# Optimization experiments

Hardware: AMD Instinct MI355X
Metric: run time of the kernel (lower is better)

The kernel has to match this reference:

```python
import jax, jax.numpy as jnp
import numpy as np

B, NQ, D, H, L, P, FFN = 32, 300, 256, 8, 3, 4, 1024
SPATIAL = [(80, 80), (40, 40), (20, 20)]  # static multi-scale feature shapes (640px, strides 8/16/32)
S = sum(h * w for h, w in SPATIAL)  # 8400
HD = D // H


def _ln(x, g, b, eps=1e-5):
    m = jnp.mean(x, -1, keepdims=True)
    v = jnp.mean((x - m) ** 2, -1, keepdims=True)
    return (x - m) * jax.lax.rsqrt(v + eps) * g + b


def _grid_sample(img, grid):
    # img: (N,C,Hh,Ww); grid: (N,Q,Pp,2) in [-1,1]; bilinear, zeros padding, align_corners=False
    N, C, Hh, Ww = img.shape
    x = (grid[..., 0] + 1.0) * (Ww * 0.5) - 0.5
    y = (grid[..., 1] + 1.0) * (Hh * 0.5) - 0.5
    x0 = jnp.floor(x)
    y0 = jnp.floor(y)
    wx1 = x - x0
    wy1 = y - y0
    x0i = x0.astype(jnp.int32)
    y0i = y0.astype(jnp.int32)
    flat = img.reshape(N, C, Hh * Ww)
    Q, Pp = grid.shape[1], grid.shape[2]

    def corner(xi, yi, w):
        valid = (xi >= 0) & (xi < Ww) & (yi >= 0) & (yi < Hh)
        idx = jnp.clip(yi, 0, Hh - 1) * Ww + jnp.clip(xi, 0, Ww - 1)
        v = jnp.take_along_axis(flat, idx.reshape(N, 1, Q * Pp), axis=2).reshape(N, C, Q, Pp)
        return v * (w * valid)[:, None]

    return (corner(x0i, y0i, (1 - wx1) * (1 - wy1))
            + corner(x0i + 1, y0i, wx1 * (1 - wy1))
            + corner(x0i, y0i + 1, (1 - wx1) * wy1)
            + corner(x0i + 1, y0i + 1, wx1 * wy1))


def setup_inputs() -> dict:
    key = jax.random.key(0)
    ks = iter(jax.random.split(key, 32))
    inp = {
        'hidden_states': jax.random.normal(next(ks), (B, NQ, D), jnp.float32),
        'position_embeddings': jax.random.normal(next(ks), (B, NQ, D), jnp.float32),
        'reference_points': jax.random.uniform(next(ks), (B, NQ, 1, 4), jnp.float32, 0.1, 0.9),
        'encoder_hidden_states': jax.random.normal(next(ks), (B, S, D), jnp.float32),
    }
    for name, shape in [('Wq', (D, D)), ('Wk', (D, D)), ('Wv', (D, D)), ('Wo', (D, D)),
                        ('Woff', (D, H * L * P * 2)), ('Waw', (D, H * L * P)),
                        ('Wval', (D, D)), ('Wout', (D, D)), ('W1', (D, FFN)), ('W2', (FFN, D))]:
        inp[name] = jax.random.normal(next(ks), shape, jnp.float32) * 0.02
    for name, dim in [('bq', D), ('bk', D), ('bv', D), ('bo', D), ('boff', H * L * P * 2),
                      ('baw', H * L * P), ('bval', D), ('bout', D), ('b1', FFN), ('b2', D)]:
        inp[name] = jnp.zeros((dim,), jnp.float32)
    for g, bname in [('ln1_g', 'ln1_b'), ('ln2_g', 'ln2_b'), ('ln3_g', 'ln3_b')]:
        inp[g] = jnp.ones((D,), jnp.float32)
        inp[bname] = jnp.zeros((D,), jnp.float32)
    return inp


def reference(hidden_states, position_embeddings, reference_points, encoder_hidden_states,
              Wq, bq, Wk, bk, Wv, bv, Wo, bo, ln1_g, ln1_b,
              Woff, boff, Waw, baw, Wval, bval, Wout, bout, ln2_g, ln2_b,
              W1, b1, W2, b2, ln3_g, ln3_b):
    hs = hidden_states
    # ---- self attention (pos-embedded q/k, raw v) ----
    hp = hs + position_embeddings
    q = ((hp @ Wq + bq) * (HD ** -0.5)).reshape(B, NQ, H, HD)
    k = (hp @ Wk + bk).reshape(B, NQ, H, HD)
    v = (hs @ Wv + bv).reshape(B, NQ, H, HD)
    attn = jax.nn.softmax(jnp.einsum('bqhd,bkhd->bhqk', q, k), axis=-1)
    sa = jnp.einsum('bhqk,bkhd->bqhd', attn, v).reshape(B, NQ, D) @ Wo + bo
    hs = _ln(hs + sa, ln1_g, ln1_b)
    # ---- multi-scale deformable cross attention ----
    hp = hs + position_embeddings
    value = (encoder_hidden_states @ Wval + bval).reshape(B, S, H, HD)
    off = (hp @ Woff + boff).reshape(B, NQ, H, L, P, 2)
    aw = jax.nn.softmax((hp @ Waw + baw).reshape(B, NQ, H, L * P), axis=-1).reshape(B, NQ, H, L, P)
    ref = reference_points  # (B,NQ,1,4) boxes -> 4-coord branch
    loc = ref[:, :, None, :, None, :2] + off / P * ref[:, :, None, :, None, 2:] * 0.5
    grids = (2.0 * loc - 1.0).transpose(0, 2, 1, 3, 4, 5).reshape(B * H, NQ, L, P, 2)
    start = 0
    samples = []
    for lvl, (hh, ww) in enumerate(SPATIAL):
        v_l = value[:, start:start + hh * ww]  # (B,hw,H,HD)
        start += hh * ww
        v_l = v_l.transpose(0, 2, 3, 1).reshape(B * H, HD, hh, ww)
        samples.append(_grid_sample(v_l, grids[:, :, lvl]))  # (B*H,HD,NQ,P)
    sampled = jnp.stack(samples, axis=3).reshape(B * H, HD, NQ, L * P)
    w = aw.transpose(0, 2, 1, 3, 4).reshape(B * H, 1, NQ, L * P)
    ca = (sampled * w).sum(-1).reshape(B, H * HD, NQ).transpose(0, 2, 1) @ Wout + bout
    hs = _ln(hs + ca, ln2_g, ln2_b)
    # ---- FFN ----
    ff = jax.nn.relu(hs @ W1 + b1) @ W2 + b2
    return _ln(hs + ff, ln3_g, ln3_b)
```

## Files before the change

kernel.cpp:

```cpp
#include <hip/hip_runtime.h>
#include <hip/hip_bf16.h>

typedef unsigned int  uint32;
typedef unsigned short ushort16;
typedef __bf16 bfx8 __attribute__((ext_vector_type(8)));
typedef float  f32x4 __attribute__((ext_vector_type(4)));

typedef __attribute__((address_space(1))) const unsigned int gas_u32;
typedef __attribute__((address_space(3))) unsigned int las_u32;

#define B_   32
#define NQ_  300
#define D_   256
#define H_   8
#define HD_  32
#define L_   3
#define P_   4
#define S_   8400
#define FFN_ 1024
#define M1   (B_*NQ_)
#define MV   (B_*S_)
#define NQP  320
#define NQT  19

__device__ inline ushort16 f2bf(float x) {
  uint32 u = __float_as_uint(x);
  uint32 r = u + 0x7fffu + ((u >> 16) & 1u);
  return (ushort16)(r >> 16);
}
__device__ inline uint32 cvtpk(float lo, float hi) {
  uint32 r; asm("v_cvt_pk_bf16_f32 %0, %1, %2" : "=v"(r) : "v"(lo), "v"(hi)); return r;
}

struct WPrep {
  const float* src[9];
  ushort16*    dst[9];
  int K[9], N[9], Npad[9], tileEnd[9];
  float scale[9];
  const float* wval; ushort16* wvalc;
  const float* bqs;  const float* bks;  float* bqk;
  const float* boffs; const float* baws; float* boffaw;
};

__global__ __launch_bounds__(256) void rt_wprep(WPrep a)
{
  __shared__ float t[32][33];
  int blk = blockIdx.x;
  if (blk < 904) {
    int wi = 0;
    while (blk >= a.tileEnd[wi]) wi++;
    int base = wi ? a.tileEnd[wi - 1] : 0;
    int idx = blk - base;
    int K = a.K[wi], N = a.N[wi];
    int ntx = a.Npad[wi] / 32;
    int n0 = (idx % ntx) * 32, k0 = (idx / ntx) * 32;
    float sc = a.scale[wi];
    const float* W = a.src[wi];
    ushort16* WT = a.dst[wi];
    int c = threadIdx.x & 31, r = threadIdx.x >> 5;
#pragma unroll
    for (int i = 0; i < 4; i++) {
      int nn = n0 + c;
      t[r + i * 8][c] = (nn < N) ? W[(size_t)(k0 + r + i * 8) * N + nn] : 0.f;
    }
    __syncthreads();
#pragma unroll
    for (int i = 0; i < 4; i++)
      WT[(size_t)(n0 + r + i * 8) * K + k0 + c] = f2bf(t[c][r + i * 8] * sc);
  } else if (blk < 936) {
    int gid = (blk - 904) * 256 + threadIdx.x;
    int c = gid >> 8, n = gid & 255;
    const float* W = a.wval;
    uint4 u;
    u.x = (uint32)f2bf(W[(c*8+0)*256 + n]) | ((uint32)f2bf(W[(c*8+1)*256 + n]) << 16);
    u.y = (uint32)f2bf(W[(c*8+2)*256 + n]) | ((uint32)f2bf(W[(c*8+3)*256 + n]) << 16);
    u.z = (uint32)f2bf(W[(c*8+4)*256 + n]) | ((uint32)f2bf(W[(c*8+5)*256 + n]) << 16);
    u.w = (uint32)f2bf(W[(c*8+6)*256 + n]) | ((uint32)f2bf(W[(c*8+7)*256 + n]) << 16);
    *(uint4*)&a.wvalc[(size_t)c * 2048 + n * 8] = u;
  } else if (blk == 936) {
    a.bqk[threadIdx.x] = a.bqs[threadIdx.x] * a.scale[0];
  } else if (blk == 937) {
    a.bqk[256 + threadIdx.x] = a.bks[threadIdx.x];
  } else if (blk == 938) {
    if (threadIdx.x < 192) a.boffaw[threadIdx.x] = a.boffs[threadIdx.x];
  } else {
    if (threadIdx.x < 96) a.boffaw[192 + threadIdx.x] = a.baws[threadIdx.x];
  }
}

__global__ __launch_bounds__(1024, 1) void rt_vgemm(
    const float* __restrict__ A, const ushort16* __restrict__ BC,
    const float* __restrict__ bias, ushort16* __restrict__ Vout)
{
  __shared__ __align__(16) char ldsB[131072];
  const int tid = threadIdx.x;
  const int lane = tid & 63, w = tid >> 6;
  const int l15 = lane & 15, l4 = lane >> 4;

#pragma unroll
  for (int i = 0; i < 8; ++i)
    __builtin_amdgcn_global_load_lds(
        (gas_u32*)(const void*)((const char*)BC + tid * 16 + i * 16384),
        (las_u32*)(void*)(&ldsB[tid * 16 + i * 16384]), 16, 0, 0);
  __syncthreads();

  const int wrow = w * 16 + l15;
  for (int t = blockIdx.x; t < MV / 256; t += 256) {
    const float* Ap = A + ((size_t)t * 256 + wrow) * 256 + l4 * 8;
    f32x4 aA = *(const f32x4*)(Ap);
    f32x4 aB = *(const f32x4*)(Ap + 4);
    f32x4 aC = *(const f32x4*)(Ap + 32);
    f32x4 aD = *(const f32x4*)(Ap + 36);
    f32x4 acc[16];
#pragma unroll
    for (int i = 0; i < 16; ++i) acc[i] = (f32x4){0.f, 0.f, 0.f, 0.f};

#pragma unroll
    for (int tt = 0; tt < 4; ++tt) {
      {
        uint4 u;
        u.x = cvtpk(aA[0], aA[1]); u.y = cvtpk(aA[2], aA[3]);
        u.z = cvtpk(aB[0], aB[1]); u.w = cvtpk(aB[2], aB[3]);
        bfx8 af = __builtin_bit_cast(bfx8, u);
        if (tt < 3) {
          aA = *(const f32x4*)(Ap + (2 * tt + 2) * 32);
          aB = *(const f32x4*)(Ap + (2 * tt + 2) * 32 + 4);
        }
        const char* bp = &ldsB[(2 * tt * 4 + l4) * 4096 + l15 * 16];
#pragma unroll
        for (int ni = 0; ni < 16; ++ni) {
          bfx8 bg = *(const bfx8*)(const void*)(bp + ni * 256);
          acc[ni] = __builtin_amdgcn_mfma_f32_16x16x32_bf16(bg, af, acc[ni], 0, 0, 0);
        }
      }
      {
        uint4 u;
        u.x = cvtpk(aC[0], aC[1]); u.y = cvtpk(aC[2], aC[3]);
        u.z = cvtpk(aD[0], aD[1]); u.w = cvtpk(aD[2], aD[3]);
        bfx8 af = __builtin_bit_cast(bfx8, u);
        if (tt < 3) {
          aC = *(const f32x4*)(Ap + (2 * tt + 3) * 32);
          aD = *(const f32x4*)(Ap + (2 * tt + 3) * 32 + 4);
        }
        const char* bp = &ldsB[((2 * tt + 1) * 4 + l4) * 4096 + l15 * 16];
#pragma unroll
        for (int ni = 0; ni < 16; ++ni) {
          bfx8 bg = *(const bfx8*)(const void*)(bp + ni * 256);
          acc[ni] = __builtin_amdgcn_mfma_f32_16x16x32_bf16(bg, af, acc[ni], 0, 0, 0);
        }
      }
    }
    int row = t * 256 + wrow;
    int bb = row / S_, s = row - bb * S_;
    ushort16* vb = Vout + (((size_t)bb * H_) * S_ + s) * HD_;
#pragma unroll
    for (int ni = 0; ni < 16; ++ni) {
      int col = ni * 16 + l4 * 4;
      f32x4 bv = *(const f32x4*)(bias + col);
      int hh = col >> 5, hd = col & 31;
      uint2 st;
      st.x = cvtpk(acc[ni][0] + bv[0], acc[ni][1] + bv[1]);
      st.y = cvtpk(acc[ni][2] + bv[2], acc[ni][3] + bv[3]);
      *(uint2*)(vb + (size_t)hh * S_ * HD_ + hd) = st;
    }
  }
}

#define GBM 128
#define GBN 128
#define GBK 32
#define LDP 40

__global__ __launch_bounds__(256) void rt_mgemm(
    const float* __restrict__ A, const float* __restrict__ A2,
    const ushort16* __restrict__ BT, const float* __restrict__ bias,
    float* __restrict__ C, float* __restrict__ C2,
    ushort16* __restrict__ Sc, ushort16* __restrict__ Sc2,
    int M, int N, int K, int klen, float scale, int mode)
{
  __shared__ __align__(16) ushort16 As[GBM][LDP];
  __shared__ __align__(16) ushort16 Bs[GBN][LDP];
  const int tid  = threadIdx.x;
  const int lane = tid & 63;
  const int w    = tid >> 6;
  const int wr   = (w >> 1) * 64;
  const int wc   = (w & 1) * 64;
  const int bm   = blockIdx.y * GBM;
  const int bn   = blockIdx.x * GBN;
  const int kz   = blockIdx.z;
  const int kb   = kz * klen;
  const int l15  = lane & 15;
  const int l4   = lane >> 4;

  f32x4 acc[4][4];
#pragma unroll
  for (int i = 0; i < 4; i++)
#pragma unroll
    for (int j = 0; j < 4; j++)
      acc[i][j] = (f32x4){0.f, 0.f, 0.f, 0.f};

  const int arow = tid >> 3, akc = tid & 7;
  const int brow = tid >> 2, bkc = tid & 3;

  for (int k0 = kb; k0 < kb + klen; k0 += GBK) {
#pragma unroll
    for (int i = 0; i < 4; i++) {
      int row = arow + i * 32;
      f32x4 v = *(const f32x4*)(A + (size_t)(bm + row) * K + k0 + akc * 4);
      if (A2) {
        f32x4 v2 = *(const f32x4*)(A2 + (size_t)(bm + row) * K + k0 + akc * 4);
#pragma unroll
        for (int r = 0; r < 4; r++) v[r] += v2[r];
      }
      uint2 u;
      u.x = cvtpk(v.x, v.y);
      u.y = cvtpk(v.z, v.w);
      *(uint2*)(&As[row][akc * 4]) = u;
    }
#pragma unroll
    for (int i = 0; i < 2; i++) {
      int row = brow + i * 64;
      uint4 v = *(const uint4*)(BT + (size_t)(bn + row) * K + k0 + bkc * 8);
      *(uint4*)(&Bs[row][bkc * 8]) = v;
    }
    __syncthreads();

    bfx8 af[4], bg[4];
#pragma unroll
    for (int mi = 0; mi < 4; mi++)
      af[mi] = *(const bfx8*)(&As[wr + mi * 16 + l15][l4 * 8]);
#pragma unroll
    for (int ni = 0; ni < 4; ni++)
      bg[ni] = *(const bfx8*)(&Bs[wc + ni * 16 + l15][l4 * 8]);
#pragma unroll
    for (int mi = 0; mi < 4; mi++)
#pragma unroll
      for (int ni = 0; ni < 4; ni++)
        acc[mi][ni] = __builtin_amdgcn_mfma_f32_16x16x32_bf16(af[mi], bg[ni], acc[mi][ni], 0, 0, 0);
    __syncthreads();
  }

  float* Cp = kz ? C2 : C;
#pragma unroll
  for (int mi = 0; mi < 4; mi++) {
#pragma unroll
    for (int ni = 0; ni < 4; ni++) {
      int col = bn + wc + ni * 16 + l15;
      if (col >= N) continue;
      float bv = kz ? 0.f : bias[col];
#pragma unroll
      for (int r = 0; r < 4; r++) {
        int row = bm + wr + mi * 16 + l4 * 4 + r;
        float vv = (acc[mi][ni][r] + bv) * scale;
        if (mode == 1) vv = fmaxf(vv, 0.f);
        if (mode == 3) {
          int bb = row / NQ_, q = row - bb * NQ_;
          int hh = col >> 5, hd = col & 31;
          Sc[(((size_t)bb * H_ + hh) * NQP + q) * HD_ + hd] = f2bf(vv);
        } else if (mode == 4) {
          int bb = row / NQ_, q = row - bb * NQ_;
          int hh = col >> 5, hd = col & 31;
          ushort16* d = (hh < 8) ? Sc : Sc2;
          d[(((size_t)bb * H_ + (hh & 7)) * NQP + q) * HD_ + hd] = f2bf(vv);
        } else {
          Cp[(size_t)row * N + col] = vv;
        }
      }
    }
  }
}

__global__ __launch_bounds__(256) void rt_vtr(const ushort16* __restrict__ vh,
                                              ushort16* __restrict__ vt)
{
  __shared__ ushort16 t[64][33];
  int bh = blockIdx.x;
  const ushort16* src = vh + (size_t)bh * NQP * HD_;
  ushort16* dst = vt + (size_t)bh * HD_ * NQP;
  int tid = threadIdx.x;
  int lrow = tid >> 2, lc8 = (tid & 3) * 8;
  int ohd = tid >> 3, oq8 = (tid & 7) * 8;
  for (int r0 = 0; r0 < NQP; r0 += 64) {
    uint4 v = *(const uint4*)(src + (size_t)(r0 + lrow) * HD_ + lc8);
    ushort16* tp = &t[lrow][lc8];
    tp[0] = (ushort16)(v.x & 0xffff); tp[1] = (ushort16)(v.x >> 16);
    tp[2] = (ushort16)(v.y & 0xffff); tp[3] = (ushort16)(v.y >> 16);
    tp[4] = (ushort16)(v.z & 0xffff); tp[5] = (ushort16)(v.z >> 16);
    tp[6] = (ushort16)(v.w & 0xffff); tp[7] = (ushort16)(v.w >> 16);
    __syncthreads();
    uint4 o;
    o.x = (uint32)t[oq8 + 0][ohd] | ((uint32)t[oq8 + 1][ohd] << 16);
    o.y = (uint32)t[oq8 + 2][ohd] | ((uint32)t[oq8 + 3][ohd] << 16);
    o.z = (uint32)t[oq8 + 4][ohd] | ((uint32)t[oq8 + 5][ohd] << 16);
    o.w = (uint32)t[oq8 + 6][ohd] | ((uint32)t[oq8 + 7][ohd] << 16);
    *(uint4*)(dst + (size_t)ohd * NQP + r0 + oq8) = o;
    __syncthreads();
  }
}

__global__ __launch_bounds__(256) void rt_fattn(
    const ushort16* __restrict__ qh, const ushort16* __restrict__ kh,
    const ushort16* __restrict__ vt, float* __restrict__ O)
{
  int gw  = blockIdx.x * 4 + (threadIdx.x >> 6);
  int bh  = gw / NQT, qt = gw - bh * NQT;
  int b   = bh >> 3, h = bh & 7;
  int lane = threadIdx.x & 63;
  int l15 = lane & 15, l4 = lane >> 4;
  int kb4 = l4 * 4;
  const ushort16* Qb = qh + (size_t)bh * NQP * HD_;
  const ushort16* Kb = kh + (size_t)bh * NQP * HD_;
  const ushort16* Vb = vt + (size_t)bh * HD_ * NQP;
  int q = qt * 16 + l15;

  bfx8 bgQ = *(const bfx8*)(const void*)(Qb + (size_t)q * HD_ + l4 * 8);
  f32x4 o0 = {0.f,0.f,0.f,0.f}, o1 = {0.f,0.f,0.f,0.f};
  float m = -1e30f, ssum = 0.f;

  for (int k0 = 0; k0 < NQP; k0 += 32) {
    bfx8 afk0 = *(const bfx8*)(const void*)(Kb + (size_t)(k0 + l15) * HD_ + l4 * 8);
    bfx8 afk1 = *(const bfx8*)(const void*)(Kb + (size_t)(k0 + 16 + l15) * HD_ + l4 * 8);
    f32x4 z = {0.f,0.f,0.f,0.f};
    f32x4 s0 = __builtin_amdgcn_mfma_f32_16x16x32_bf16(afk0, bgQ, z, 0, 0, 0);
    f32x4 s1 = __builtin_amdgcn_mfma_f32_16x16x32_bf16(afk1, bgQ, z, 0, 0, 0);
    int ka = k0 + kb4, kbb = k0 + 16 + kb4;
#pragma unroll
    for (int r = 0; r < 4; r++) {
      if (ka  + r >= NQ_) s0[r] = -1e30f;
      if (kbb + r >= NQ_) s1[r] = -1e30f;
    }
    float cm = fmaxf(fmaxf(fmaxf(s0[0], s0[1]), fmaxf(s0[2], s0[3])),
                     fmaxf(fmaxf(s1[0], s1[1]), fmaxf(s1[2], s1[3])));
    cm = fmaxf(cm, __shfl_xor(cm, 16));
    cm = fmaxf(cm, __shfl_xor(cm, 32));
    float nm = fmaxf(m, cm);
    float sc = __expf(m - nm);
    m = nm;
    f32x4 p0, p1;
#pragma unroll
    for (int r = 0; r < 4; r++) { p0[r] = __expf(s0[r] - m); p1[r] = __expf(s1[r] - m); }
    float ls = (p0[0]+p0[1]+p0[2]+p0[3]) + (p1[0]+p1[1]+p1[2]+p1[3]);
    ls += __shfl_xor(ls, 16);
    ls += __shfl_xor(ls, 32);
    ssum = ssum * sc + ls;

    uint32 t0w0 = cvtpk(p0[0], p0[1]);
    uint32 t0w1 = cvtpk(p0[2], p0[3]);
    uint32 t1w0 = cvtpk(p1[0], p1[1]);
    uint32 t1w1 = cvtpk(p1[2], p1[3]);
    int srcA = l15 + 32 * (l4 & 1);
    int srcB = srcA + 16;
    uint32 a00 = __shfl((int)t0w0, srcA), a01 = __shfl((int)t0w1, srcA);
    uint32 b00 = __shfl((int)t0w0, srcB), b01 = __shfl((int)t0w1, srcB);
    uint32 a10 = __shfl((int)t1w0, srcA), a11 = __shfl((int)t1w1, srcA);
    uint32 b10 = __shfl((int)t1w0, srcB), b11 = __shfl((int)t1w1, srcB);
    bool hi = (l4 >= 2);
    uint4 pw;
    pw.x = hi ? a10 : a00;
    pw.y = hi ? a11 : a01;
    pw.z = hi ? b10 : b00;
    pw.w = hi ? b11 : b01;
    bfx8 bgP = __builtin_bit_cast(bfx8, pw);

    bfx8 afv0 = *(const bfx8*)(const void*)(Vb + (size_t)l15 * NQP + k0 + l4 * 8);
    bfx8 afv1 = *(const bfx8*)(const void*)(Vb + (size_t)(16 + l15) * NQP + k0 + l4 * 8);
#pragma unroll
    for (int r = 0; r < 4; r++) { o0[r] *= sc; o1[r] *= sc; }
    o0 = __builtin_amdgcn_mfma_f32_16x16x32_bf16(afv0, bgP, o0, 0, 0, 0);
    o1 = __builtin_amdgcn_mfma_f32_16x16x32_bf16(afv1, bgP, o1, 0, 0, 0);
  }

  if (q < NQ_) {
    float inv = 1.f / ssum;
    float* op = O + ((size_t)(b * NQ_ + q)) * D_ + h * HD_ + kb4;
    f32x4 r0, r1;
#pragma unroll
    for (int r = 0; r < 4; r++) { r0[r] = o0[r] * inv; r1[r] = o1[r] * inv; }
    *(f32x4*)op = r0;
    *(f32x4*)(op + 16) = r1;
  }
}

__global__ __launch_bounds__(256) void rt_ln2(
    const float* __restrict__ X, const float* __restrict__ R1,
    const float* __restrict__ R2,
    const float* __restrict__ g, const float* __restrict__ be,
    float* __restrict__ O, int rows)
{
  int row = blockIdx.x * 4 + (threadIdx.x >> 6);
  int lane = threadIdx.x & 63;
  if (row >= rows) return;
  size_t base = (size_t)row * D_ + lane * 4;
  float4 x = *(const float4*)(X + base);
  float4 r = *(const float4*)(R1 + base);
  float v0 = x.x + r.x, v1 = x.y + r.y, v2 = x.z + r.z, v3 = x.w + r.w;
  if (R2) {
    float4 r2 = *(const float4*)(R2 + base);
    v0 += r2.x; v1 += r2.y; v2 += r2.z; v3 += r2.w;
  }
  float s = v0 + v1 + v2 + v3;
  float sq = v0*v0 + v1*v1 + v2*v2 + v3*v3;
#pragma unroll
  for (int o = 32; o >= 1; o >>= 1) { s += __shfl_xor(s, o); sq += __shfl_xor(sq, o); }
  float mean = s * (1.f / D_);
  float var  = sq * (1.f / D_) - mean * mean;
  float inv  = 1.f / sqrtf(var + 1e-5f);
  int c = lane * 4;
  float4 gv = *(const float4*)(g + c);
  float4 bv = *(const float4*)(be + c);
  float4 o4;
  o4.x = (v0 - mean) * inv * gv.x + bv.x;
  o4.y = (v1 - mean) * inv * gv.y + bv.y;
  o4.z = (v2 - mean) * inv * gv.z + bv.z;
  o4.w = (v3 - mean) * inv * gv.w + bv.w;
  *(float4*)(O + base) = o4;
}

__device__ inline void rt_acc8(const ushort16* p, float wgt, float* acc) {
  uint4 v = *(const uint4*)(const void*)p;
  acc[0] += wgt * __uint_as_float(v.x << 16);
  acc[1] += wgt * __uint_as_float(v.x & 0xffff0000u);
  acc[2] += wgt * __uint_as_float(v.y << 16);
  acc[3] += wgt * __uint_as_float(v.y & 0xffff0000u);
  acc[4] += wgt * __uint_as_float(v.z << 16);
  acc[5] += wgt * __uint_as_float(v.z & 0xffff0000u);
  acc[6] += wgt * __uint_as_float(v.w << 16);
  acc[7] += wgt * __uint_as_float(v.w & 0xffff0000u);
}

__global__ __launch_bounds__(256) void rt_deform(
    const ushort16* __restrict__ value,
    const float* __restrict__ offaw,
    const float* __restrict__ ref,
    float* __restrict__ O)
{
  int gid = blockIdx.x * 256 + threadIdx.x;
  int hd0 = (gid & 3) * 8;
  int bqh = gid >> 2;
  int h   = bqh & 7;
  int bq  = bqh >> 3;
  int b   = bq / NQ_;
  const float* rp = ref + (size_t)bq * 4;
  float rx = rp[0], ry = rp[1];
  float rw = rp[2] * 0.125f, rh = rp[3] * 0.125f;
  const float* op = offaw + (size_t)bq * 288 + h * 24;
  const float* ap = offaw + (size_t)bq * 288 + 192 + h * 12;
  float e[12]; float mx = -1e30f;
#pragma unroll
  for (int i = 0; i < 12; i++) { e[i] = ap[i]; mx = fmaxf(mx, e[i]); }
  float ssum = 0.f;
#pragma unroll
  for (int i = 0; i < 12; i++) { e[i] = __expf(e[i] - mx); ssum += e[i]; }
  float sinv = 1.f / ssum;

  const ushort16* vb = value + ((size_t)b * H_ + h) * (size_t)S_ * HD_ + hd0;
  float acc[8];
#pragma unroll
  for (int i = 0; i < 8; i++) acc[i] = 0.f;
  const int starts[3] = {0, 6400, 8000};
  const int dims[3]   = {80, 40, 20};
#pragma unroll
  for (int l = 0; l < L_; l++) {
    const int Wl = dims[l];
    const ushort16* vl = vb + (size_t)starts[l] * HD_;
#pragma unroll
    for (int p = 0; p < P_; p++) {
      int ip = l * P_ + p;
      float wgt = e[ip] * sinv;
      float x = (rx + op[ip*2+0] * rw) * Wl - 0.5f;
      float y = (ry + op[ip*2+1] * rh) * Wl - 0.5f;
      float x0f = floorf(x), y0f = floorf(y);
      int   x0 = (int)x0f,  y0 = (int)y0f;
      float wx1 = x - x0f, wy1 = y - y0f;
      float wx0 = 1.f - wx1, wy0 = 1.f - wy1;
      bool xok0 = (x0 >= 0) & (x0 < Wl), xok1 = (x0+1 >= 0) & (x0+1 < Wl);
      bool yok0 = (y0 >= 0) & (y0 < Wl), yok1 = (y0+1 >= 0) & (y0+1 < Wl);
      const ushort16* r0p = vl + (size_t)(y0 * Wl) * HD_;
      const ushort16* r1p = r0p + (size_t)Wl * HD_;
      if (xok0 & yok0) rt_acc8(r0p + (size_t)x0 * HD_,     wgt * wx0 * wy0, acc);
      if (xok1 & yok0) rt_acc8(r0p + (size_t)(x0+1) * HD_, wgt * wx1 * wy0, acc);
      if (xok0 & yok1) rt_acc8(r1p + (size_t)x0 * HD_,     wgt * wx0 * wy1, acc);
      if (xok1 & yok1) rt_acc8(r1p + (size_t)(x0+1) * HD_, wgt * wx1 * wy1, acc);
    }
  }
  float* outp = O + (size_t)bq * D_ + h * HD_ + hd0;
  float4 a0, a1;
  a0.x = acc[0]; a0.y = acc[1]; a0.z = acc[2]; a0.w = acc[3];
  a1.x = acc[4]; a1.y = acc[5]; a1.z = acc[6]; a1.w = acc[7];
  *(float4*)outp = a0;
  *(float4*)(outp + 4) = a1;
}

extern "C" void kernel_launch(void* const* d_in, const int* in_sizes, int n_in,
                              void* d_out, int out_size, void* d_ws, size_t ws_size,
                              hipStream_t stream)
{
  const float* hs   = (const float*)d_in[0];
  const float* pos  = (const float*)d_in[1];
  const float* ref  = (const float*)d_in[2];
  const float* ehs  = (const float*)d_in[3];
  const float* Wq   = (const float*)d_in[4];
  const float* Wk   = (const float*)d_in[5];
  const float* Wv   = (const float*)d_in[6];
  const float* Wo   = (const float*)d_in[7];
  const float* Woff = (const float*)d_in[8];
  const float* Waw  = (const float*)d_in[9];
  const float* Wval = (const float*)d_in[10];
  const float* Wout = (const float*)d_in[11];
  const float* W1   = (const float*)d_in[12];
  const float* W2   = (const float*)d_in[13];
  const float* bq   = (const float*)d_in[14];
  const float* bk   = (const float*)d_in[15];
  const float* bvv  = (const float*)d_in[16];
  const float* bo   = (const float*)d_in[17];
  const float* boff = (const float*)d_in[18];
  const float* baw  = (const float*)d_in[19];
  const float* bval = (const float*)d_in[20];
  const float* bout = (const float*)d_in[21];
  const float* b1   = (const float*)d_in[22];
  const float* b2   = (const float*)d_in[23];
  const float* ln1g = (const float*)d_in[24];
  const float* ln1b = (const float*)d_in[25];
  const float* ln2g = (const float*)d_in[26];
  const float* ln2b = (const float*)d_in[27];
  const float* ln3g = (const float*)d_in[28];
  const float* ln3b = (const float*)d_in[29];
  float* out = (float*)d_out;

  float* ws = (float*)d_ws;
  ushort16* value = (ushort16*)ws;
  float* t2     = ws + 34406400;
  float* t0     = ws + 36864000;
  float* t1     = ws + 39321600;
  float* hs1    = ws + 41779200;
  float* hs2    = ws + 44236800;
  float* offawb = ws + 46694400;
  float* ffn1   = ws + 49459200;
  ushort16* qh = (ushort16*)(ws + 59289600);
  ushort16* kh = (ushort16*)(ws + 60600320);
  ushort16* vh = (ushort16*)(ws + 61911040);
  ushort16* vt = (ushort16*)(ws + 63221760);
  ushort16* wbase  = (ushort16*)(ws + 64532480);
  ushort16* WqkT   = wbase;
  ushort16* WvT    = WqkT   + 131072;
  ushort16* WoT    = WvT    + 65536;
  ushort16* WoffawT= WoT    + 65536;
  ushort16* WoutT  = WoffawT+ 98304;
  ushort16* W1T    = WoutT  + 65536;
  ushort16* W2T    = W1T    + 262144;
  ushort16* WvalC  = W2T    + 262144;
  float* bqk    = (float*)(WvalC + 65536);
  float* boffaw = bqk + 512;

  const float qscale = 0.17677669529663687f;

  WPrep a;
  a.src[0]=Wq;   a.dst[0]=WqkT;            a.K[0]=256;  a.N[0]=256;  a.Npad[0]=256; a.scale[0]=qscale;
  a.src[1]=Wk;   a.dst[1]=WqkT+65536;      a.K[1]=256;  a.N[1]=256;  a.Npad[1]=256; a.scale[1]=1.f;
  a.src[2]=Wv;   a.dst[2]=WvT;             a.K[2]=256;  a.N[2]=256;  a.Npad[2]=256; a.scale[2]=1.f;
  a.src[3]=Wo;   a.dst[3]=WoT;             a.K[3]=256;  a.N[3]=256;  a.Npad[3]=256; a.scale[3]=1.f;
  a.src[4]=Woff; a.dst[4]=WoffawT;         a.K[4]=256;  a.N[4]=192;  a.Npad[4]=192; a.scale[4]=1.f;
  a.src[5]=Waw;  a.dst[5]=WoffawT+49152;   a.K[5]=256;  a.N[5]=96;   a.Npad[5]=96;  a.scale[5]=1.f;
  a.src[6]=Wout; a.dst[6]=WoutT;           a.K[6]=256;  a.N[6]=256;  a.Npad[6]=256; a.scale[6]=1.f;
  a.src[7]=W1;   a.dst[7]=W1T;             a.K[7]=256;  a.N[7]=1024; a.Npad[7]=1024;a.scale[7]=1.f;
  a.src[8]=W2;   a.dst[8]=W2T;             a.K[8]=1024; a.N[8]=256;  a.Npad[8]=256; a.scale[8]=1.f;
  int cum = 0;
  int tiles[9] = {64, 64, 64, 64, 48, 24, 64, 256, 256};
  for (int i = 0; i < 9; i++) { cum += tiles[i]; a.tileEnd[i] = cum; }
  a.wval = Wval; a.wvalc = WvalC;
  a.bqs = bq; a.bks = bk; a.bqk = bqk;
  a.boffs = boff; a.baws = baw; a.boffaw = boffaw;
  rt_wprep<<<dim3(940), 256, 0, stream>>>(a);

  rt_vgemm<<<dim3(256), 1024, 0, stream>>>(ehs, WvalC, bval, value);

  rt_mgemm<<<dim3(4, M1/GBM, 1), 256, 0, stream>>>(hs, pos, WqkT, bqk, nullptr, nullptr, qh, kh, M1, 512, 256, 256, 1.f, 4);
  rt_mgemm<<<dim3(2, M1/GBM, 1), 256, 0, stream>>>(hs, nullptr, WvT, bvv, nullptr, nullptr, vh, nullptr, M1, 256, 256, 256, 1.f, 3);
  rt_vtr<<<dim3(B_*H_), 256, 0, stream>>>(vh, vt);
  rt_fattn<<<dim3(B_*H_*NQT/4), 256, 0, stream>>>(qh, kh, vt, t0);
  rt_mgemm<<<dim3(2, M1/GBM, 2), 256, 0, stream>>>(t0, nullptr, WoT, bo, t1, t2, nullptr, nullptr, M1, 256, 256, 128, 1.f, 0);
  rt_ln2<<<dim3(M1/4), 256, 0, stream>>>(hs, t1, t2, ln1g, ln1b, hs1, M1);
  rt_mgemm<<<dim3(3, M1/GBM, 1), 256, 0, stream>>>(hs1, pos, WoffawT, boffaw, offawb, nullptr, nullptr, nullptr, M1, 288, 256, 256, 1.f, 0);
  rt_deform<<<dim3(M1*H_*4/256), 256, 0, stream>>>(value, offawb, ref, t0);
  rt_mgemm<<<dim3(2, M1/GBM, 2), 256, 0, stream>>>(t0, nullptr, WoutT, bout, t1, t2, nullptr, nullptr, M1, 256, 256, 128, 1.f, 0);
  rt_ln2<<<dim3(M1/4), 256, 0, stream>>>(hs1, t1, t2, ln2g, ln2b, hs2, M1);
  rt_mgemm<<<dim3(8, M1/GBM, 1), 256, 0, stream>>>(hs2, nullptr, W1T, b1, ffn1, nullptr, nullptr, nullptr, M1, FFN_, 256, 256, 1.f, 1);
  rt_mgemm<<<dim3(2, M1/GBM, 2), 256, 0, stream>>>(ffn1, nullptr, W2T, b2, t1, t2, nullptr, nullptr, M1, 256, 1024, 512, 1.f, 0);
  rt_ln2<<<dim3(M1/4), 256, 0, stream>>>(hs2, t1, t2, ln3g, ln3b, out, M1);
}
```

Before: 394.1 us.

## Prefetch next value-GEMM tile, split deform sampling in two, drop split-K GEMMs

The value-projection GEMM now loads the first A tile before the barrier and prefetches the next tile's A rows during the current tile's last MFMA steps, so global loads overlap compute across tiles. The deformable sampling kernel is split into two halves of six sampling points each, written to two buffers, which doubles the thread count for this latency-bound gather. The following output projection sums the halves through its A2 input. The split-K path of the generic GEMM is removed, so the projection and FFN GEMMs run with full K in one block and rt_ln2 receives a null second partial. This cuts grid parallelism for those GEMMs and relies on rt_ln2 handling a null pointer.

```diff
diff --git a/kernel.cpp b/kernel.cpp
--- a/kernel.cpp
+++ b/kernel.cpp
@@ -102,54 +102,50 @@
     __builtin_amdgcn_global_load_lds(
         (gas_u32*)(const void*)((const char*)BC + tid * 16 + i * 16384),
         (las_u32*)(void*)(&ldsB[tid * 16 + i * 16384]), 16, 0, 0);
+
+  const int wrow = w * 16 + l15;
+  const float* Abase = A + (size_t)wrow * 256 + l4 * 8;
+
+  f32x4 P0x, P0y, P1x, P1y, P2x, P2y, P3x, P3y;
+  {
+    const float* At = Abase + (size_t)blockIdx.x * 65536;
+    P0x = *(const f32x4*)(At +   0); P0y = *(const f32x4*)(At +   4);
+    P1x = *(const f32x4*)(At +  32); P1y = *(const f32x4*)(At +  36);
+    P2x = *(const f32x4*)(At +  64); P2y = *(const f32x4*)(At +  68);
+    P3x = *(const f32x4*)(At +  96); P3y = *(const f32x4*)(At + 100);
+  }
   __syncthreads();
 
-  const int wrow = w * 16 + l15;
+#define VSTEP(PX, PY, ts, nl, cond) { \
+    uint4 u_; \
+    u_.x = cvtpk(PX[0], PX[1]); u_.y = cvtpk(PX[2], PX[3]); \
+    u_.z = cvtpk(PY[0], PY[1]); u_.w = cvtpk(PY[2], PY[3]); \
+    bfx8 af_ = __builtin_bit_cast(bfx8, u_); \
+    if (cond) { PX = *(const f32x4*)(nl); PY = *(const f32x4*)((nl) + 4); } \
+    const char* bp_ = &ldsB[((ts) * 4 + l4) * 4096 + l15 * 16]; \
+    _Pragma("unroll") \
+    for (int ni = 0; ni < 16; ++ni) { \
+      bfx8 bg_ = *(const bfx8*)(const void*)(bp_ + ni * 256); \
+      acc[ni] = __builtin_amdgcn_mfma_f32_16x16x32_bf16(bg_, af_, acc[ni], 0, 0, 0); \
+    } }
+
   for (int t = blockIdx.x; t < MV / 256; t += 256) {
-    const float* Ap = A + ((size_t)t * 256 + wrow) * 256 + l4 * 8;
-    f32x4 aA = *(const f32x4*)(Ap);
-    f32x4 aB = *(const f32x4*)(Ap + 4);
-    f32x4 aC = *(const f32x4*)(Ap + 32);
-    f32x4 aD = *(const f32x4*)(Ap + 36);
+    const float* At = Abase + (size_t)t * 65536;
+    const float* An = Abase + (size_t)(t + 256) * 65536;
+    const bool more = (t + 256) < MV / 256;
     f32x4 acc[16];
 #pragma unroll
     for (int i = 0; i < 16; ++i) acc[i] = (f32x4){0.f, 0.f, 0.f, 0.f};
 
-#pragma unroll
-    for (int tt = 0; tt < 4; ++tt) {
-      {
-        uint4 u;
-        u.x = cvtpk(aA[0], aA[1]); u.y = cvtpk(aA[2], aA[3]);
-        u.z = cvtpk(aB[0], aB[1]); u.w = cvtpk(aB[2], aB[3]);
-        bfx8 af = __builtin_bit_cast(bfx8, u);
-        if (tt < 3) {
-          aA = *(const f32x4*)(Ap + (2 * tt + 2) * 32);
-          aB = *(const f32x4*)(Ap + (2 * tt + 2) * 32 + 4);
-        }
-        const char* bp = &ldsB[(2 * tt * 4 + l4) * 4096 + l15 * 16];
-#pragma unroll
-        for (int ni = 0; ni < 16; ++ni) {
-          bfx8 bg = *(const bfx8*)(const void*)(bp + ni * 256);
-          acc[ni] = __builtin_amdgcn_mfma_f32_16x16x32_bf16(bg, af, acc[ni], 0, 0, 0);
-        }
-      }
-      {
-        uint4 u;
-        u.x = cvtpk(aC[0], aC[1]); u.y = cvtpk(aC[2], aC[3]);
-        u.z = cvtpk(aD[0], aD[1]); u.w = cvtpk(aD[2], aD[3]);
-        bfx8 af = __builtin_bit_cast(bfx8, u);
-        if (tt < 3) {
-          aC = *(const f32x4*)(Ap + (2 * tt + 3) * 32);
-          aD = *(const f32x4*)(Ap + (2 * tt + 3) * 32 + 4);
-        }
-        const char* bp = &ldsB[((2 * tt + 1) * 4 + l4) * 4096 + l15 * 16];
-#pragma unroll
-        for (int ni = 0; ni < 16; ++ni) {
-          bfx8 bg = *(const bfx8*)(const void*)(bp + ni * 256);
-          acc[ni] = __builtin_amdgcn_mfma_f32_16x16x32_bf16(bg, af, acc[ni], 0, 0, 0);
-        }
-      }
-    }
+    VSTEP(P0x, P0y, 0, At + 128, true)
+    VSTEP(P1x, P1y, 1, At + 160, true)
+    VSTEP(P2x, P2y, 2, At + 192, true)
+    VSTEP(P3x, P3y, 3, At + 224, true)
+    VSTEP(P0x, P0y, 4, An +   0, more)
+    VSTEP(P1x, P1y, 5, An +  32, more)
+    VSTEP(P2x, P2y, 6, An +  64, more)
+    VSTEP(P3x, P3y, 7, An +  96, more)
+
     int row = t * 256 + wrow;
     int bb = row / S_, s = row - bb * S_;
     ushort16* vb = Vout + (((size_t)bb * H_) * S_ + s) * HD_;
@@ -164,6 +160,7 @@
       *(uint2*)(vb + (size_t)hh * S_ * HD_ + hd) = st;
     }
   }
+#undef VSTEP
 }
 
 #define GBM 128
@@ -174,9 +171,9 @@
 __global__ __launch_bounds__(256) void rt_mgemm(
     const float* __restrict__ A, const float* __restrict__ A2,
     const ushort16* __restrict__ BT, const float* __restrict__ bias,
-    float* __restrict__ C, float* __restrict__ C2,
+    float* __restrict__ C,
     ushort16* __restrict__ Sc, ushort16* __restrict__ Sc2,
-    int M, int N, int K, int klen, float scale, int mode)
+    int M, int N, int K, float scale, int mode)
 {
   __shared__ __align__(16) ushort16 As[GBM][LDP];
   __shared__ __align__(16) ushort16 Bs[GBN][LDP];
@@ -187,8 +184,6 @@
   const int wc   = (w & 1) * 64;
   const int bm   = blockIdx.y * GBM;
   const int bn   = blockIdx.x * GBN;
-  const int kz   = blockIdx.z;
-  const int kb   = kz * klen;
   const int l15  = lane & 15;
   const int l4   = lane >> 4;
 
@@ -202,7 +197,7 @@
   const int arow = tid >> 3, akc = tid & 7;
   const int brow = tid >> 2, bkc = tid & 3;
 
-  for (int k0 = kb; k0 < kb + klen; k0 += GBK) {
+  for (int k0 = 0; k0 < K; k0 += GBK) {
 #pragma unroll
     for (int i = 0; i < 4; i++) {
       int row = arow + i * 32;
@@ -240,14 +235,13 @@
     __syncthreads();
   }
 
-  float* Cp = kz ? C2 : C;
 #pragma unroll
   for (int mi = 0; mi < 4; mi++) {
 #pragma unroll
     for (int ni = 0; ni < 4; ni++) {
       int col = bn + wc + ni * 16 + l15;
       if (col >= N) continue;
-      float bv = kz ? 0.f : bias[col];
+      float bv = bias[col];
 #pragma unroll
       for (int r = 0; r < 4; r++) {
         int row = bm + wr + mi * 16 + l4 * 4 + r;
@@ -263,7 +257,7 @@
           ushort16* d = (hh < 8) ? Sc : Sc2;
           d[(((size_t)bb * H_ + (hh & 7)) * NQP + q) * HD_ + hd] = f2bf(vv);
         } else {
-          Cp[(size_t)row * N + col] = vv;
+          C[(size_t)row * N + col] = vv;
         }
       }
     }
@@ -432,9 +426,11 @@
     const ushort16* __restrict__ value,
     const float* __restrict__ offaw,
     const float* __restrict__ ref,
-    float* __restrict__ O)
-{
-  int gid = blockIdx.x * 256 + threadIdx.x;
+    float* __restrict__ O1, float* __restrict__ O2)
+{
+  const int NBLK = (M1 * H_ * 4) / 256;
+  int g = (blockIdx.x >= NBLK) ? 1 : 0;
+  int gid = (blockIdx.x - g * NBLK) * 256 + threadIdx.x;
   int hd0 = (gid & 3) * 8;
   int bqh = gid >> 2;
   int h   = bqh & 7;
@@ -457,33 +453,31 @@
   float acc[8];
 #pragma unroll
   for (int i = 0; i < 8; i++) acc[i] = 0.f;
-  const int starts[3] = {0, 6400, 8000};
-  const int dims[3]   = {80, 40, 20};
-#pragma unroll
-  for (int l = 0; l < L_; l++) {
-    const int Wl = dims[l];
-    const ushort16* vl = vb + (size_t)starts[l] * HD_;
-#pragma unroll
-    for (int p = 0; p < P_; p++) {
-      int ip = l * P_ + p;
-      float wgt = e[ip] * sinv;
-      float x = (rx + op[ip*2+0] * rw) * Wl - 0.5f;
-      float y = (ry + op[ip*2+1] * rh) * Wl - 0.5f;
-      float x0f = floorf(x), y0f = floorf(y);
-      int   x0 = (int)x0f,  y0 = (int)y0f;
-      float wx1 = x - x0f, wy1 = y - y0f;
-      float wx0 = 1.f - wx1, wy0 = 1.f - wy1;
-      bool xok0 = (x0 >= 0) & (x0 < Wl), xok1 = (x0+1 >= 0) & (x0+1 < Wl);
-      bool yok0 = (y0 >= 0) & (y0 < Wl), yok1 = (y0+1 >= 0) & (y0+1 < Wl);
-      const ushort16* r0p = vl + (size_t)(y0 * Wl) * HD_;
-      const ushort16* r1p = r0p + (size_t)Wl * HD_;
-      if (xok0 & yok0) rt_acc8(r0p + (size_t)x0 * HD_,     wgt * wx0 * wy0, acc);
-      if (xok1 & yok0) rt_acc8(r0p + (size_t)(x0+1) * HD_, wgt * wx1 * wy0, acc);
-      if (xok0 & yok1) rt_acc8(r1p + (size_t)x0 * HD_,     wgt * wx0 * wy1, acc);
-      if (xok1 & yok1) rt_acc8(r1p + (size_t)(x0+1) * HD_, wgt * wx1 * wy1, acc);
-    }
-  }
-  float* outp = O + (size_t)bq * D_ + h * HD_ + hd0;
+  const int p0 = g * 6;
+#pragma unroll
+  for (int j = 0; j < 6; ++j) {
+    int ip = p0 + j;
+    int lvl = ip >> 2;
+    int Wl = (lvl == 0) ? 80 : ((lvl == 1) ? 40 : 20);
+    int st = (lvl == 0) ? 0 : ((lvl == 1) ? 6400 : 8000);
+    const ushort16* vl = vb + (size_t)st * HD_;
+    float wgt = e[ip] * sinv;
+    float x = (rx + op[ip*2+0] * rw) * Wl - 0.5f;
+    float y = (ry + op[ip*2+1] * rh) * Wl - 0.5f;
+    float x0f = floorf(x), y0f = floorf(y);
+    int   x0 = (int)x0f,  y0 = (int)y0f;
+    float wx1 = x - x0f, wy1 = y - y0f;
+    float wx0 = 1.f - wx1, wy0 = 1.f - wy1;
+    bool xok0 = (x0 >= 0) & (x0 < Wl), xok1 = (x0+1 >= 0) & (x0+1 < Wl);
+    bool yok0 = (y0 >= 0) & (y0 < Wl), yok1 = (y0+1 >= 0) & (y0+1 < Wl);
+    const ushort16* r0p = vl + (size_t)(y0 * Wl) * HD_;
+    const ushort16* r1p = r0p + (size_t)Wl * HD_;
+    if (xok0 & yok0) rt_acc8(r0p + (size_t)x0 * HD_,     wgt * wx0 * wy0, acc);
+    if (xok1 & yok0) rt_acc8(r0p + (size_t)(x0+1) * HD_, wgt * wx1 * wy0, acc);
+    if (xok0 & yok1) rt_acc8(r1p + (size_t)x0 * HD_,     wgt * wx0 * wy1, acc);
+    if (xok1 & yok1) rt_acc8(r1p + (size_t)(x0+1) * HD_, wgt * wx1 * wy1, acc);
+  }
+  float* outp = (g ? O2 : O1) + (size_t)bq * D_ + h * HD_ + hd0;
   float4 a0, a1;
   a0.x = acc[0]; a0.y = acc[1]; a0.z = acc[2]; a0.w = acc[3];
   a1.x = acc[4]; a1.y = acc[5]; a1.z = acc[6]; a1.w = acc[7];
@@ -574,17 +568,17 @@
 
   rt_vgemm<<<dim3(256), 1024, 0, stream>>>(ehs, WvalC, bval, value);
 
-  rt_mgemm<<<dim3(4, M1/GBM, 1), 256, 0, stream>>>(hs, pos, WqkT, bqk, nullptr, nullptr, qh, kh, M1, 512, 256, 256, 1.f, 4);
-  rt_mgemm<<<dim3(2, M1/GBM, 1), 256, 0, stream>>>(hs, nullptr, WvT, bvv, nullptr, nullptr, vh, nullptr, M1, 256, 256, 256, 1.f, 3);
+  rt_mgemm<<<dim3(4, M1/GBM), 256, 0, stream>>>(hs, pos, WqkT, bqk, nullptr, qh, kh, M1, 512, 256, 1.f, 4);
+  rt_mgemm<<<dim3(2, M1/GBM), 256, 0, stream>>>(hs, nullptr, WvT, bvv, nullptr, vh, nullptr, M1, 256, 256, 1.f, 3);
   rt_vtr<<<dim3(B_*H_), 256, 0, stream>>>(vh, vt);
   rt_fattn<<<dim3(B_*H_*NQT/4), 256, 0, stream>>>(qh, kh, vt, t0);
-  rt_mgemm<<<dim3(2, M1/GBM, 2), 256, 0, stream>>>(t0, nullptr, WoT, bo, t1, t2, nullptr, nullptr, M1, 256, 256, 128, 1.f, 0);
-  rt_ln2<<<dim3(M1/4), 256, 0, stream>>>(hs, t1, t2, ln1g, ln1b, hs1, M1);
-  rt_mgemm<<<dim3(3, M1/GBM, 1), 256, 0, stream>>>(hs1, pos, WoffawT, boffaw, offawb, nullptr, nullptr, nullptr, M1, 288, 256, 256, 1.f, 0);
-  rt_deform<<<dim3(M1*H_*4/256), 256, 0, stream>>>(value, offawb, ref, t0);
-  rt_mgemm<<<dim3(2, M1/GBM, 2), 256, 0, stream>>>(t0, nullptr, WoutT, bout, t1, t2, nullptr, nullptr, M1, 256, 256, 128, 1.f, 0);
-  rt_ln2<<<dim3(M1/4), 256, 0, stream>>>(hs1, t1, t2, ln2g, ln2b, hs2, M1);
-  rt_mgemm<<<dim3(8, M1/GBM, 1), 256, 0, stream>>>(hs2, nullptr, W1T, b1, ffn1, nullptr, nullptr, nullptr, M1, FFN_, 256, 256, 1.f, 1);
-  rt_mgemm<<<dim3(2, M1/GBM, 2), 256, 0, stream>>>(ffn1, nullptr, W2T, b2, t1, t2, nullptr, nullptr, M1, 256, 1024, 512, 1.f, 0);
-  rt_ln2<<<dim3(M1/4), 256, 0, stream>>>(hs2, t1, t2, ln3g, ln3b, out, M1);
-}
+  rt_mgemm<<<dim3(2, M1/GBM), 256, 0, stream>>>(t0, nullptr, WoT, bo, t1, nullptr, nullptr, M1, 256, 256, 1.f, 0);
+  rt_ln2<<<dim3(M1/4), 256, 0, stream>>>(hs, t1, nullptr, ln1g, ln1b, hs1, M1);
+  rt_mgemm<<<dim3(3, M1/GBM), 256, 0, stream>>>(hs1, pos, WoffawT, boffaw, offawb, nullptr, nullptr, M1, 288, 256, 1.f, 0);
+  rt_deform<<<dim3(M1*H_*4*2/256), 256, 0, stream>>>(value, offawb, ref, t0, t2);
+  rt_mgemm<<<dim3(2, M1/GBM), 256, 0, stream>>>(t0, t2, WoutT, bout, t1, nullptr, nullptr, M1, 256, 256, 1.f, 0);
+  rt_ln2<<<dim3(M1/4), 256, 0, stream>>>(hs1, t1, nullptr, ln2g, ln2b, hs2, M1);
+  rt_mgemm<<<dim3(8, M1/GBM), 256, 0, stream>>>(hs2, nullptr, W1T, b1, ffn1, nullptr, nullptr, M1, FFN_, 256, 1.f, 1);
+  rt_mgemm<<<dim3(2, M1/GBM), 256, 0, stream>>>(ffn1, nullptr, W2T, b2, t1, nullptr, nullptr, M1, 256, 1024, 1.f, 0);
+  rt_ln2<<<dim3(M1/4), 256, 0, stream>>>(hs2, t1, nullptr, ln3g, ln3b, out, M1);
+}
```

Result: slower. 442.7 us (+12.3%).
